# Optimization experiments

Measured on AMD Instinct MI355X. Metric: run time of the kernel, lower is better.

Reference implementation:

```python
import jax, jax.numpy as jnp
import numpy as np

B, H, W = 16, 128, 128
NUM_SAMPLES, HID = 16, 256


def setup_inputs() -> dict:
    key = jax.random.key(0)
    ks = jax.random.split(key, 12)
    inp = {
        "x": jax.random.uniform(ks[0], (B, H, W, 2), jnp.float32) * 2.0 - 1.0,
        "sample_idx": jax.random.randint(ks[1], (B,), 0, NUM_SAMPLES),
        "shift_vectors": jax.random.normal(ks[2], (NUM_SAMPLES, 2), jnp.float32) * 0.05,
        "rotation_angle": jax.random.normal(ks[3], (NUM_SAMPLES, 1), jnp.float32) * 0.05,
        "color_scales": 1.0 + jax.random.normal(ks[4], (NUM_SAMPLES, 3), jnp.float32) * 0.05,
        "color_shifts": jax.random.normal(ks[5], (NUM_SAMPLES, 3), jnp.float32) * 0.05,
        "W1": jax.random.normal(ks[6], (2, HID), jnp.float32) / np.sqrt(2.0),
        "b1": jnp.zeros((HID,), jnp.float32),
        "W2": jax.random.normal(ks[7], (HID, HID), jnp.float32) / np.sqrt(HID),
        "b2": jnp.zeros((HID,), jnp.float32),
        "W3": jax.random.normal(ks[8], (HID, HID), jnp.float32) / np.sqrt(HID),
        "b3": jnp.zeros((HID,), jnp.float32),
        "W4": jax.random.normal(ks[9], (HID, 3), jnp.float32) / np.sqrt(HID),
        "b4": jnp.zeros((3,), jnp.float32),
    }
    return inp


def reference(x, sample_idx, shift_vectors, rotation_angle, color_scales, color_shifts,
              W1, b1, W2, b2, W3, b3, W4, b4):
    # Per-sample affine coordinate transform (vectorized gather + batched 2x3 affine).
    shift = shift_vectors[sample_idx]            # [B,2] -> (dy, dx)
    dy, dx = shift[:, 0], shift[:, 1]
    ang = rotation_angle[sample_idx, 0]          # [B]
    c, s = jnp.cos(ang), jnp.sin(ang)
    rot = jnp.stack([jnp.stack([c, -s], -1),
                     jnp.stack([s, c], -1)], -2)  # [B,2,2]
    trans = jnp.stack([dx, dy], -1)               # [B,2]
    coords = jnp.einsum('bij,bhwj->bhwi', rot, x) + trans[:, None, None, :]

    # INR decoder MLP: coords -> RGB
    h = jax.nn.relu(coords @ W1 + b1)
    h = jax.nn.relu(h @ W2 + b2)
    h = jax.nn.relu(h @ W3 + b3)
    out = h @ W4 + b4                             # [B,H,W,3]

    # Per-sample color affine, skipped for reference sample idx==0.
    scales = color_scales[sample_idx][:, None, None, :]
    shifts = color_shifts[sample_idx][:, None, None, :]
    mask = (sample_idx != 0)[:, None, None, None]
    out = jnp.where(mask, out * scales + shifts, out)
    return out, dx, dy
```

## Files before the change

kernel.cpp:

```cpp
#include <hip/hip_runtime.h>
#include <math.h>

typedef _Float16 half8  __attribute__((ext_vector_type(8)));
typedef _Float16 half4v __attribute__((ext_vector_type(4)));
typedef float    f32x4  __attribute__((ext_vector_type(4)));
typedef float    f32x2  __attribute__((ext_vector_type(2)));
typedef float    f32x16 __attribute__((ext_vector_type(16)));

#define W1OFF 0
#define W2OFF 4096
#define W3OFF 69632
#define W4OFF 135168
#define SWTOT 139264
#define OUT_PIX (16*128*128)

__global__ void inr_prep(const float* __restrict__ W1, const float* __restrict__ W2,
                         const float* __restrict__ W3, const float* __restrict__ W4,
                         const int* __restrict__ sidx, const float* __restrict__ sv,
                         _Float16* __restrict__ wsw, float* __restrict__ outtail)
{
    int tid = blockIdx.x * 256 + threadIdx.x;
    if (tid < 16) {
        int si = sidx[tid];
        outtail[tid]      = sv[2*si + 1];
        outtail[16 + tid] = sv[2*si + 0];
    }
    if (tid >= SWTOT) return;
    int kind, rel;
    if      (tid < W2OFF) { kind = 0; rel = tid; }
    else if (tid < W3OFF) { kind = 1; rel = tid - W2OFF; }
    else if (tid < W4OFF) { kind = 2; rel = tid - W3OFF; }
    else                  { kind = 3; rel = tid - W4OFF; }
    int j    = rel & 7;
    int lane = (rel >> 3) & 63;
    int blk  = rel >> 9;
    float val;
    if (kind == 3) {
        int q = lane >> 4, ln = lane & 15;
        int m = ln;
        int k = blk * 32 + q * 8 + j;
        val = (m < 3) ? W4[k*3 + m] : 0.0f;
    } else {
        int hi = lane >> 5, lo = lane & 31;
        if (kind == 0) {
            int m = blk*32 + lo;
            int k = hi*8 + j;
            val = (k < 2) ? W1[k*256 + m] : 0.0f;
        } else {
            int MT = blk & 7, kk = blk >> 3;
            int m = MT*32 + lo;
            int k = kk*16 + hi*8 + j;
            val = (kind == 1) ? W2[k*256 + m] : W3[k*256 + m];
        }
    }
    wsw[tid] = (_Float16)val;
}

template<int NKK>
__device__ __forceinline__ void do_layer32(const half8* __restrict__ Asw,
                                           const float* __restrict__ bias,
                                           _Float16* hbuf, int w, int lane)
{
    int lo = lane & 31, hi = lane >> 5;
    f32x16 acc[2][4];
#pragma unroll
    for (int mt = 0; mt < 2; ++mt)
#pragma unroll
        for (int nt = 0; nt < 4; ++nt)
#pragma unroll
            for (int r = 0; r < 16; ++r)
                acc[mt][nt][r] = 0.f;

#pragma unroll
    for (int kk = 0; kk < NKK; ++kk) {
        half8 aw[2];
#pragma unroll
        for (int mt = 0; mt < 2; ++mt)
            aw[mt] = Asw[(kk*8 + 2*w + mt)*64 + lane];
        half8 bf[4];
        int g = kk*2 + hi;
#pragma unroll
        for (int nt = 0; nt < 4; ++nt)
            bf[nt] = *(const half8*)&hbuf[g*1024 + (32*nt + lo)*8];
#pragma unroll
        for (int nt = 0; nt < 4; ++nt)
#pragma unroll
            for (int mt = 0; mt < 2; ++mt)
                acc[mt][nt] = __builtin_amdgcn_mfma_f32_32x32x16_f16(aw[mt], bf[nt], acc[mt][nt], 0, 0, 0);
    }
    __syncthreads();
#pragma unroll
    for (int mt = 0; mt < 2; ++mt) {
        int MT = 2*w + mt;
#pragma unroll
        for (int gi = 0; gi < 4; ++gi) {
            int hid0 = MT*32 + gi*8 + 4*hi;
            f32x4 bv = *(const f32x4*)&bias[hid0];
#pragma unroll
            for (int nt = 0; nt < 4; ++nt) {
                int px = 32*nt + lo;
                half4v hv;
                hv[0] = (_Float16)fmaxf(acc[mt][nt][gi*4+0] + bv[0], 0.f);
                hv[1] = (_Float16)fmaxf(acc[mt][nt][gi*4+1] + bv[1], 0.f);
                hv[2] = (_Float16)fmaxf(acc[mt][nt][gi*4+2] + bv[2], 0.f);
                hv[3] = (_Float16)fmaxf(acc[mt][nt][gi*4+3] + bv[3], 0.f);
                *(half4v*)&hbuf[(MT*4 + gi)*1024 + px*8 + 4*hi] = hv;
            }
        }
    }
    __syncthreads();
}

__launch_bounds__(256, 2)
__global__ void inr_fused(const float* __restrict__ x, const int* __restrict__ sidx_p,
                          const float* __restrict__ sv, const float* __restrict__ ra,
                          const float* __restrict__ cs, const float* __restrict__ csh,
                          const float* __restrict__ b1, const float* __restrict__ b2,
                          const float* __restrict__ b3, const float* __restrict__ b4,
                          const _Float16* __restrict__ wsw, float* __restrict__ out)
{
    __shared__ __align__(16) _Float16 hbuf[32768];
    int t = threadIdx.x;
    int lane = t & 63, w = t >> 6, q = lane >> 4, ln = lane & 15;
    int pixbase = blockIdx.x * 128;
    int b = pixbase >> 14;
    int sidx = sidx_p[b];
    float dy = sv[2*sidx], dx = sv[2*sidx + 1];
    float ang = ra[sidx];
    float sn, cn;
    sincosf(ang, &sn, &cn);

    if (t < 128) {
        int p = t;
        f32x2 xv = *(const f32x2*)&x[(pixbase + p)*2];
        float u = cn*xv[0] - sn*xv[1] + dx;
        float v = sn*xv[0] + cn*xv[1] + dy;
        half8 z;
#pragma unroll
        for (int i = 0; i < 8; ++i) z[i] = (_Float16)0.0f;
        z[0] = (_Float16)u; z[1] = (_Float16)v;
        *(half8*)&hbuf[0*1024 + p*8] = z;
    } else {
        int p = t - 128;
        half8 z;
#pragma unroll
        for (int i = 0; i < 8; ++i) z[i] = (_Float16)0.0f;
        *(half8*)&hbuf[1*1024 + p*8] = z;
    }
    __syncthreads();

    const half8* wsw8 = (const half8*)wsw;
    do_layer32<1>(wsw8,                b1, hbuf, w, lane);
    do_layer32<16>(wsw8 + (W2OFF >> 3), b2, hbuf, w, lane);
    do_layer32<16>(wsw8 + (W3OFF >> 3), b3, hbuf, w, lane);

    const half8* w4p = wsw8 + (W4OFF >> 3);
    f32x4 a4[2];
    a4[0] = (f32x4){0.f,0.f,0.f,0.f};
    a4[1] = (f32x4){0.f,0.f,0.f,0.f};
#pragma unroll
    for (int kkb = 0; kkb < 8; ++kkb) {
        half8 aw = w4p[kkb*64 + lane];
#pragma unroll
        for (int i = 0; i < 2; ++i) {
            int pixel = 16*(2*w + i) + ln;
            half8 bf = *(const half8*)&hbuf[(kkb*4 + q)*1024 + pixel*8];
            a4[i] = __builtin_amdgcn_mfma_f32_16x16x32_f16(aw, bf, a4[i], 0, 0, 0);
        }
    }
    if (q == 0) {
        bool doc = (sidx != 0);
        float s0 = cs[sidx*3+0], s1 = cs[sidx*3+1], s2 = cs[sidx*3+2];
        float t0 = csh[sidx*3+0], t1 = csh[sidx*3+1], t2 = csh[sidx*3+2];
        float bb0 = b4[0], bb1 = b4[1], bb2 = b4[2];
#pragma unroll
        for (int i = 0; i < 2; ++i) {
            int gp = pixbase + 16*(2*w + i) + ln;
            float v0 = a4[i][0] + bb0;
            float v1 = a4[i][1] + bb1;
            float v2 = a4[i][2] + bb2;
            if (doc) { v0 = v0*s0 + t0; v1 = v1*s1 + t1; v2 = v2*s2 + t2; }
            out[gp*3 + 0] = v0;
            out[gp*3 + 1] = v1;
            out[gp*3 + 2] = v2;
        }
    }
}

extern "C" void kernel_launch(void* const* d_in, const int* in_sizes, int n_in,
                              void* d_out, int out_size, void* d_ws, size_t ws_size,
                              hipStream_t stream)
{
    const float* x    = (const float*)d_in[0];
    const int*   sidx = (const int*)  d_in[1];
    const float* sv   = (const float*)d_in[2];
    const float* ra   = (const float*)d_in[3];
    const float* cs   = (const float*)d_in[4];
    const float* csh  = (const float*)d_in[5];
    const float* W1   = (const float*)d_in[6];
    const float* b1   = (const float*)d_in[7];
    const float* W2   = (const float*)d_in[8];
    const float* b2   = (const float*)d_in[9];
    const float* W3   = (const float*)d_in[10];
    const float* b3   = (const float*)d_in[11];
    const float* W4   = (const float*)d_in[12];
    const float* b4   = (const float*)d_in[13];
    float* out = (float*)d_out;
    _Float16* wsw = (_Float16*)d_ws;

    inr_prep<<<SWTOT/256, 256, 0, stream>>>(W1, W2, W3, W4, sidx, sv, wsw, out + OUT_PIX*3);
    inr_fused<<<OUT_PIX/128, 256, 0, stream>>>(x, sidx, sv, ra, cs, csh,
                                               b1, b2, b3, b4, wsw, out);
}
```

Baseline: 144.9 us.

## Consume own-written hidden chunks before the barrier to overlap layer epilogue

Each wave writes a fixed slice of the shared hidden buffer in its epilogue. It now starts the next layer's K loop on exactly that slice before the block-wide barrier, then syncs and processes the remaining K chunks in a rotated order. The trailing barrier after each layer's epilogue becomes a compiler memory fence only, and the final small layer is split the same way. This hides part of the barrier wait behind MFMA work, but depends on an exact match between write ownership and read chunks, and changes the accumulation order.

```diff
diff --git a/kernel.cpp b/kernel.cpp
--- a/kernel.cpp
+++ b/kernel.cpp
@@ -56,7 +56,7 @@
     wsw[tid] = (_Float16)val;
 }
 
-template<int NKK>
+template<int NOWN, int NKK>
 __device__ __forceinline__ void do_layer32(const half8* __restrict__ Asw,
                                            const float* __restrict__ bias,
                                            _Float16* hbuf, int w, int lane)
@@ -71,24 +71,38 @@
             for (int r = 0; r < 16; ++r)
                 acc[mt][nt][r] = 0.f;
 
-#pragma unroll
-    for (int kk = 0; kk < NKK; ++kk) {
-        half8 aw[2];
-#pragma unroll
-        for (int mt = 0; mt < 2; ++mt)
-            aw[mt] = Asw[(kk*8 + 2*w + mt)*64 + lane];
-        half8 bf[4];
-        int g = kk*2 + hi;
-#pragma unroll
-        for (int nt = 0; nt < 4; ++nt)
-            bf[nt] = *(const half8*)&hbuf[g*1024 + (32*nt + lo)*8];
-#pragma unroll
-        for (int nt = 0; nt < 4; ++nt)
-#pragma unroll
-            for (int mt = 0; mt < 2; ++mt)
-                acc[mt][nt] = __builtin_amdgcn_mfma_f32_32x32x16_f16(aw[mt], bf[nt], acc[mt][nt], 0, 0, 0);
-    }
+#define KKBODY(KK)                                                              \
+    {                                                                           \
+        int kk = (KK);                                                          \
+        half8 aw[2];                                                            \
+        _Pragma("unroll")                                                       \
+        for (int mt = 0; mt < 2; ++mt)                                          \
+            aw[mt] = Asw[(kk*8 + 2*w + mt)*64 + lane];                          \
+        half8 bf[4];                                                            \
+        int g = kk*2 + hi;                                                      \
+        _Pragma("unroll")                                                       \
+        for (int nt = 0; nt < 4; ++nt)                                          \
+            bf[nt] = *(const half8*)&hbuf[g*1024 + (32*nt + lo)*8];             \
+        _Pragma("unroll")                                                       \
+        for (int nt = 0; nt < 4; ++nt)                                          \
+            _Pragma("unroll")                                                   \
+            for (int mt = 0; mt < 2; ++mt)                                      \
+                acc[mt][nt] = __builtin_amdgcn_mfma_f32_32x32x16_f16(aw[mt], bf[nt], acc[mt][nt], 0, 0, 0); \
+    }
+
+#pragma unroll
+    for (int i = 0; i < NOWN; ++i)
+        KKBODY((4*w + i) & (NKK - 1));
+
     __syncthreads();
+
+#pragma unroll
+    for (int i = NOWN; i < NKK; ++i)
+        KKBODY(NOWN ? ((4*w + i) & (NKK - 1)) : i);
+
+    __syncthreads();
+#undef KKBODY
+
 #pragma unroll
     for (int mt = 0; mt < 2; ++mt) {
         int MT = 2*w + mt;
@@ -108,7 +122,7 @@
             }
         }
     }
-    __syncthreads();
+    asm volatile("" ::: "memory");
 }
 
 __launch_bounds__(256, 2)
@@ -147,27 +161,36 @@
         for (int i = 0; i < 8; ++i) z[i] = (_Float16)0.0f;
         *(half8*)&hbuf[1*1024 + p*8] = z;
     }
-    __syncthreads();
 
     const half8* wsw8 = (const half8*)wsw;
-    do_layer32<1>(wsw8,                b1, hbuf, w, lane);
-    do_layer32<16>(wsw8 + (W2OFF >> 3), b2, hbuf, w, lane);
-    do_layer32<16>(wsw8 + (W3OFF >> 3), b3, hbuf, w, lane);
+    do_layer32<0,1>(wsw8,                 b1, hbuf, w, lane);
+    do_layer32<4,16>(wsw8 + (W2OFF >> 3), b2, hbuf, w, lane);
+    do_layer32<4,16>(wsw8 + (W3OFF >> 3), b3, hbuf, w, lane);
 
     const half8* w4p = wsw8 + (W4OFF >> 3);
     f32x4 a4[2];
     a4[0] = (f32x4){0.f,0.f,0.f,0.f};
     a4[1] = (f32x4){0.f,0.f,0.f,0.f};
-#pragma unroll
-    for (int kkb = 0; kkb < 8; ++kkb) {
-        half8 aw = w4p[kkb*64 + lane];
-#pragma unroll
-        for (int i = 0; i < 2; ++i) {
-            int pixel = 16*(2*w + i) + ln;
-            half8 bf = *(const half8*)&hbuf[(kkb*4 + q)*1024 + pixel*8];
-            a4[i] = __builtin_amdgcn_mfma_f32_16x16x32_f16(aw, bf, a4[i], 0, 0, 0);
-        }
-    }
+#define K4BODY(KKB)                                                             \
+    {                                                                           \
+        int kkb = (KKB);                                                        \
+        half8 aw = w4p[kkb*64 + lane];                                          \
+        _Pragma("unroll")                                                       \
+        for (int i = 0; i < 2; ++i) {                                           \
+            int pixel = 16*(2*w + i) + ln;                                      \
+            half8 bf = *(const half8*)&hbuf[(kkb*4 + q)*1024 + pixel*8];        \
+            a4[i] = __builtin_amdgcn_mfma_f32_16x16x32_f16(aw, bf, a4[i], 0, 0, 0); \
+        }                                                                       \
+    }
+#pragma unroll
+    for (int j = 0; j < 2; ++j)
+        K4BODY(2*w + j);
+    __syncthreads();
+#pragma unroll
+    for (int j = 2; j < 8; ++j)
+        K4BODY((2*w + j) & 7);
+#undef K4BODY
+
     if (q == 0) {
         bool doc = (sidx != 0);
         float s0 = cs[sidx*3+0], s1 = cs[sidx*3+1], s2 = cs[sidx*3+2];
```

After: 147.0 us. About the same (+1.4%).

## Keep layer activations in registers and overlap own-slice MFMAs with LDS writes

Applied to the files above, without the earlier changes.

The layer epilogue now converts each wave's accumulators straight into B-operand fragments in registers, using permlane32_swap plus relu and fp16 packing. Each wave runs the K-slices it produced itself (phase1) from those registers while the fragments are being written to LDS. It then syncs and reads the remaining slices from LDS in a rotated order (phase2). Bias is folded into the accumulator init, and the extra barrier before the writeback is gone. The aim is fewer LDS round-trips and barrier stalls, at the cost of higher register pressure from holding the 16 fragments alongside the accumulators, which could spill under launch bounds of 2.

```diff
diff --git a/kernel.cpp b/kernel.cpp
--- a/kernel.cpp
+++ b/kernel.cpp
@@ -3,9 +3,12 @@
 
 typedef _Float16 half8  __attribute__((ext_vector_type(8)));
 typedef _Float16 half4v __attribute__((ext_vector_type(4)));
+typedef _Float16 half2v __attribute__((ext_vector_type(2)));
 typedef float    f32x4  __attribute__((ext_vector_type(4)));
 typedef float    f32x2  __attribute__((ext_vector_type(2)));
 typedef float    f32x16 __attribute__((ext_vector_type(16)));
+typedef int      int2v  __attribute__((ext_vector_type(2)));
+typedef int      int4v  __attribute__((ext_vector_type(4)));
 
 #define W1OFF 0
 #define W2OFF 4096
@@ -56,23 +59,81 @@
     wsw[tid] = (_Float16)val;
 }
 
-template<int NKK>
-__device__ __forceinline__ void do_layer32(const half8* __restrict__ Asw,
-                                           const float* __restrict__ bias,
-                                           _Float16* hbuf, int w, int lane)
+
+__device__ __forceinline__ int pack_relu(float a, float b)
+{
+    half2v hp;
+    hp[0] = (_Float16)fmaxf(a, 0.f);
+    hp[1] = (_Float16)fmaxf(b, 0.f);
+    return __builtin_bit_cast(int, hp);
+}
+
+__device__ __forceinline__ void make_frags(const f32x16 (&acc)[2][4], half8 (&F)[4][4])
+{
+#pragma unroll
+    for (int i = 0; i < 4; ++i) {
+        int ms = i >> 1, e = i & 1;
+#pragma unroll
+        for (int nt = 0; nt < 4; ++nt) {
+            int w0 = pack_relu(acc[ms][nt][8*e+0], acc[ms][nt][8*e+1]);
+            int w1 = pack_relu(acc[ms][nt][8*e+2], acc[ms][nt][8*e+3]);
+            int w2 = pack_relu(acc[ms][nt][8*e+4], acc[ms][nt][8*e+5]);
+            int w3 = pack_relu(acc[ms][nt][8*e+6], acc[ms][nt][8*e+7]);
+            int2v r02 = __builtin_amdgcn_permlane32_swap(w0, w2, false, false);
+            int2v r13 = __builtin_amdgcn_permlane32_swap(w1, w3, false, false);
+            int4v fw;
+            fw[0] = r02[0];
+            fw[1] = r13[0];
+            fw[2] = r02[1];
+            fw[3] = r13[1];
+            F[i][nt] = __builtin_bit_cast(half8, fw);
+        }
+    }
+}
+
+__device__ __forceinline__ void bias_init(f32x16 (&acc)[2][4], const float* __restrict__ bias,
+                                          int w, int hi)
+{
+#pragma unroll
+    for (int mt = 0; mt < 2; ++mt)
+#pragma unroll
+        for (int m = 0; m < 4; ++m) {
+            f32x4 bv = *(const f32x4*)&bias[64*w + 32*mt + 8*m + 4*hi];
+#pragma unroll
+            for (int nt = 0; nt < 4; ++nt)
+#pragma unroll
+                for (int c = 0; c < 4; ++c)
+                    acc[mt][nt][4*m+c] = bv[c];
+        }
+}
+
+__device__ __forceinline__ void phase1(const half8* __restrict__ Asw,
+                                       f32x16 (&acc)[2][4], const half8 (&F)[4][4],
+                                       int w, int lane)
+{
+#pragma unroll
+    for (int i = 0; i < 4; ++i) {
+        int kk = 4*w + i;
+        half8 aw[2];
+#pragma unroll
+        for (int mt = 0; mt < 2; ++mt)
+            aw[mt] = Asw[(kk*8 + 2*w + mt)*64 + lane];
+#pragma unroll
+        for (int nt = 0; nt < 4; ++nt)
+#pragma unroll
+            for (int mt = 0; mt < 2; ++mt)
+                acc[mt][nt] = __builtin_amdgcn_mfma_f32_32x32x16_f16(aw[mt], F[i][nt], acc[mt][nt], 0, 0, 0);
+    }
+}
+
+__device__ __forceinline__ void phase2(const half8* __restrict__ Asw,
+                                       f32x16 (&acc)[2][4], const _Float16* __restrict__ hbuf,
+                                       int w, int lane)
 {
     int lo = lane & 31, hi = lane >> 5;
-    f32x16 acc[2][4];
-#pragma unroll
-    for (int mt = 0; mt < 2; ++mt)
-#pragma unroll
-        for (int nt = 0; nt < 4; ++nt)
-#pragma unroll
-            for (int r = 0; r < 16; ++r)
-                acc[mt][nt][r] = 0.f;
-
-#pragma unroll
-    for (int kk = 0; kk < NKK; ++kk) {
+#pragma unroll
+    for (int idx = 0; idx < 12; ++idx) {
+        int kk = (4*w + 4 + idx) & 15;
         half8 aw[2];
 #pragma unroll
         for (int mt = 0; mt < 2; ++mt)
@@ -88,27 +149,17 @@
             for (int mt = 0; mt < 2; ++mt)
                 acc[mt][nt] = __builtin_amdgcn_mfma_f32_32x32x16_f16(aw[mt], bf[nt], acc[mt][nt], 0, 0, 0);
     }
-    __syncthreads();
-#pragma unroll
-    for (int mt = 0; mt < 2; ++mt) {
-        int MT = 2*w + mt;
-#pragma unroll
-        for (int gi = 0; gi < 4; ++gi) {
-            int hid0 = MT*32 + gi*8 + 4*hi;
-            f32x4 bv = *(const f32x4*)&bias[hid0];
-#pragma unroll
-            for (int nt = 0; nt < 4; ++nt) {
-                int px = 32*nt + lo;
-                half4v hv;
-                hv[0] = (_Float16)fmaxf(acc[mt][nt][gi*4+0] + bv[0], 0.f);
-                hv[1] = (_Float16)fmaxf(acc[mt][nt][gi*4+1] + bv[1], 0.f);
-                hv[2] = (_Float16)fmaxf(acc[mt][nt][gi*4+2] + bv[2], 0.f);
-                hv[3] = (_Float16)fmaxf(acc[mt][nt][gi*4+3] + bv[3], 0.f);
-                *(half4v*)&hbuf[(MT*4 + gi)*1024 + px*8 + 4*hi] = hv;
-            }
-        }
-    }
-    __syncthreads();
+}
+
+__device__ __forceinline__ void write_frags(_Float16* hbuf, const half8 (&F)[4][4],
+                                            int w, int lane)
+{
+    int lo = lane & 31, hi = lane >> 5;
+#pragma unroll
+    for (int i = 0; i < 4; ++i)
+#pragma unroll
+        for (int nt = 0; nt < 4; ++nt)
+            *(half8*)&hbuf[(8*w + 2*i + hi)*1024 + (32*nt + lo)*8] = F[i][nt];
 }
 
 __launch_bounds__(256, 2)
@@ -122,6 +173,7 @@
     __shared__ __align__(16) _Float16 hbuf[32768];
     int t = threadIdx.x;
     int lane = t & 63, w = t >> 6, q = lane >> 4, ln = lane & 15;
+    int lo = lane & 31, hi = lane >> 5;
     int pixbase = blockIdx.x * 128;
     int b = pixbase >> 14;
     int sidx = sidx_p[b];
@@ -150,9 +202,46 @@
     __syncthreads();
 
     const half8* wsw8 = (const half8*)wsw;
-    do_layer32<1>(wsw8,                b1, hbuf, w, lane);
-    do_layer32<16>(wsw8 + (W2OFF >> 3), b2, hbuf, w, lane);
-    do_layer32<16>(wsw8 + (W3OFF >> 3), b3, hbuf, w, lane);
+    f32x16 acc[2][4];
+    half8 F[4][4];
+
+    bias_init(acc, b1, w, hi);
+    {
+        half8 aw[2];
+#pragma unroll
+        for (int mt = 0; mt < 2; ++mt)
+            aw[mt] = wsw8[(2*w + mt)*64 + lane];
+        half8 bf[4];
+#pragma unroll
+        for (int nt = 0; nt < 4; ++nt)
+            bf[nt] = *(const half8*)&hbuf[hi*1024 + (32*nt + lo)*8];
+#pragma unroll
+        for (int nt = 0; nt < 4; ++nt)
+#pragma unroll
+            for (int mt = 0; mt < 2; ++mt)
+                acc[mt][nt] = __builtin_amdgcn_mfma_f32_32x32x16_f16(aw[mt], bf[nt], acc[mt][nt], 0, 0, 0);
+    }
+    make_frags(acc, F);
+    __syncthreads();
+
+    bias_init(acc, b2, w, hi);
+    write_frags(hbuf, F, w, lane);
+    phase1(wsw8 + (W2OFF >> 3), acc, F, w, lane);
+    __syncthreads();
+    phase2(wsw8 + (W2OFF >> 3), acc, hbuf, w, lane);
+    make_frags(acc, F);
+    __syncthreads();
+
+    bias_init(acc, b3, w, hi);
+    write_frags(hbuf, F, w, lane);
+    phase1(wsw8 + (W3OFF >> 3), acc, F, w, lane);
+    __syncthreads();
+    phase2(wsw8 + (W3OFF >> 3), acc, hbuf, w, lane);
+    make_frags(acc, F);
+    __syncthreads();
+
+    write_frags(hbuf, F, w, lane);
+    __syncthreads();
 
     const half8* w4p = wsw8 + (W4OFF >> 3);
     f32x4 a4[2];
```

After: 151.6 us. +4.6%, slower.
